# Kernel optimization log

Hardware: AMD Instinct MI355X
Metric: run time of the kernel (lower is better)

Reference implementation:

```python
import jax, jax.numpy as jnp
import numpy as np

N, K, P = 40000, 32, 15
C = 128            # output_feature_dim (kpconv in/out channels)
H_POS, D_POS = 64, 256
H_AGG, D_PROC = 256, 256
RADIUS = 1.0
KP_EXTENT = RADIUS / (P ** (1.0 / 3.0) - 1.0) * 1.5
SLOPE = 0.01       # nn.LeakyReLU default
EPS = 1e-5         # BatchNorm1d default eps


def _lin(key, din, dout):
    k1, k2 = jax.random.split(key)
    lim = 1.0 / np.sqrt(din)
    w = jax.random.uniform(k1, (din, dout), minval=-lim, maxval=lim, dtype=jnp.float32)
    b = jax.random.uniform(k2, (dout,), minval=-lim, maxval=lim, dtype=jnp.float32)
    return w, b


def _bn(x, g, b):
    # BatchNorm1d in training mode: biased batch statistics
    m = jnp.mean(x, axis=0)
    v = jnp.var(x, axis=0)
    return (x - m) * jax.lax.rsqrt(v + EPS) * g + b


def _lrelu(x):
    return jnp.where(x >= 0, x, SLOPE * x)


def setup_inputs() -> dict:
    key = jax.random.key(0)
    ks = jax.random.split(key, 16)
    inp = {}
    inp['points'] = jax.random.normal(ks[0], (N, 3), dtype=jnp.float32) * 10.0
    inp['covariances'] = jax.random.normal(ks[1], (N, 9), dtype=jnp.float32)
    inp['neighbors_index'] = jax.random.randint(ks[2], (N, K), 0, N)
    inp['pre_w'], inp['pre_b'] = _lin(ks[3], 9, C)
    inp['pre_bn_g'] = jnp.ones((C,), jnp.float32); inp['pre_bn_b'] = jnp.zeros((C,), jnp.float32)
    kp = jax.random.normal(ks[4], (P, 3), dtype=jnp.float32)
    kp = kp / jnp.linalg.norm(kp, axis=1, keepdims=True)
    inp['kernel_points'] = kp * jax.random.uniform(ks[5], (P, 1), dtype=jnp.float32) * RADIUS
    inp['kp_weights'] = jax.random.normal(ks[6], (P, C, C), dtype=jnp.float32) * (1.0 / np.sqrt(P * C))
    inp['pos_w1'], inp['pos_b1'] = _lin(ks[7], 3, H_POS)
    inp['pos_bn1_g'] = jnp.ones((H_POS,), jnp.float32); inp['pos_bn1_b'] = jnp.zeros((H_POS,), jnp.float32)
    inp['pos_w2'], inp['pos_b2'] = _lin(ks[8], H_POS, D_POS)
    inp['pos_bn2_g'] = jnp.ones((D_POS,), jnp.float32); inp['pos_bn2_b'] = jnp.zeros((D_POS,), jnp.float32)
    inp['agg_w1'], inp['agg_b1'] = _lin(ks[9], C, H_AGG)
    inp['agg_bn1_g'] = jnp.ones((H_AGG,), jnp.float32); inp['agg_bn1_b'] = jnp.zeros((H_AGG,), jnp.float32)
    inp['agg_w2'], inp['agg_b2'] = _lin(ks[10], H_AGG, D_PROC)
    inp['agg_bn2_g'] = jnp.ones((D_PROC,), jnp.float32); inp['agg_bn2_b'] = jnp.zeros((D_PROC,), jnp.float32)
    inp['keep_w1'], inp['keep_b1'] = _lin(ks[11], D_PROC, D_PROC // 4)
    inp['keep_bn_g'] = jnp.ones((D_PROC // 4,), jnp.float32); inp['keep_bn_b'] = jnp.zeros((D_PROC // 4,), jnp.float32)
    inp['keep_w2'], inp['keep_b2'] = _lin(ks[12], D_PROC // 4, 1)
    du = D_PROC + D_POS
    inp['uniq_w1'], inp['uniq_b1'] = _lin(ks[13], du, du // 4)
    inp['uniq_bn_g'] = jnp.ones((du // 4,), jnp.float32); inp['uniq_bn_b'] = jnp.zeros((du // 4,), jnp.float32)
    inp['uniq_w2'], inp['uniq_b2'] = _lin(ks[14], du // 4, 1)
    return inp


def reference(points, covariances, neighbors_index,
              pre_w, pre_b, pre_bn_g, pre_bn_b,
              kernel_points, kp_weights,
              pos_w1, pos_b1, pos_bn1_g, pos_bn1_b,
              pos_w2, pos_b2, pos_bn2_g, pos_bn2_b,
              agg_w1, agg_b1, agg_bn1_g, agg_bn1_b,
              agg_w2, agg_b2, agg_bn2_g, agg_bn2_b,
              keep_w1, keep_b1, keep_bn_g, keep_bn_b, keep_w2, keep_b2,
              uniq_w1, uniq_b1, uniq_bn_g, uniq_bn_b, uniq_w2, uniq_b2):
    # preactivation on 9-dim flattened covariances
    features = _lrelu(_bn(covariances @ pre_w + pre_b, pre_bn_g, pre_bn_b))  # [N, C]

    # ---- rigid KPConv (linear influence, sum aggregation, shadow point at index N) ----
    s_pad = jnp.concatenate([points, jnp.full((1, 3), 1e6, points.dtype)], axis=0)
    x_pad = jnp.concatenate([features, jnp.zeros((1, C), features.dtype)], axis=0)
    nb = s_pad[neighbors_index] - points[:, None, :]                          # [N, K, 3]
    # squared distances to kernel points without materializing [N,K,P,3]
    sq = (jnp.sum(nb * nb, -1)[:, :, None]
          + jnp.sum(kernel_points * kernel_points, -1)[None, None, :]
          - 2.0 * jnp.einsum('nkd,pd->nkp', nb, kernel_points))               # [N, K, P]
    infl = jnp.maximum(1.0 - jnp.sqrt(jnp.maximum(sq, 0.0)) / KP_EXTENT, 0.0)  # [N, K, P]
    nx = x_pad[neighbors_index]                                               # [N, K, C]
    weighted = jnp.einsum('nkp,nkc->npc', infl, nx)                           # [N, P, C]
    conv = jnp.einsum('npc,pcd->nd', weighted, kp_weights)                    # [N, C]
    # density normalization: count non-shadow neighbors
    nnum = jnp.maximum(jnp.sum(jnp.sum(nx, -1) > 0.0, axis=-1), 1)
    kpconv_feature = conv / nnum[:, None].astype(conv.dtype)

    # position embedding MLP
    pos = _lrelu(_bn(points @ pos_w1 + pos_b1, pos_bn1_g, pos_bn1_b))
    pos = _lrelu(_bn(pos @ pos_w2 + pos_b2, pos_bn2_g, pos_bn2_b))            # [N, 256]

    # feature aggregation MLP
    agg = _lrelu(_bn(kpconv_feature @ agg_w1 + agg_b1, agg_bn1_g, agg_bn1_b))
    agg = _lrelu(_bn(agg @ agg_w2 + agg_b2, agg_bn2_g, agg_bn2_b))            # [N, 256]

    # heads
    kh = _lrelu(_bn(agg @ keep_w1 + keep_b1, keep_bn_g, keep_bn_b))
    match_score = jax.nn.sigmoid((kh @ keep_w2 + keep_b2).ravel())
    u_in = jnp.concatenate([pos, agg], axis=1)                                # [N, 512]
    uh = _lrelu(_bn(u_in @ uniq_w1 + uniq_b1, uniq_bn_g, uniq_bn_b))
    unique_score = jax.nn.sigmoid((uh @ uniq_w2 + uniq_b2).ravel())
    return match_score, unique_score, neighbors_index
```

## Files before the change

kernel.cpp:

```cpp
#include <hip/hip_runtime.h>
#include <math.h>


#define NPTS 40000
#define KNB  32
#define PKP  15
#define SLOPE 0.01f
#define BNEPS 1e-5f
#define INV_N (1.0f/40000.0f)

typedef __attribute__((ext_vector_type(8))) short bf16x8;
typedef __attribute__((ext_vector_type(4))) float f32x4;

__device__ __forceinline__ float lrelu(float x){ return x >= 0.0f ? x : SLOPE*x; }
__device__ __forceinline__ unsigned short f2bf(float f){
  unsigned int b = __float_as_uint(f);
  b += 0x7fffu + ((b>>16)&1u);
  return (unsigned short)(b>>16);
}
__device__ __forceinline__ float bf2f(unsigned short u){
  return __uint_as_float(((unsigned int)u)<<16);
}


__global__ __launch_bounds__(256) void k_prep(
    const float* __restrict__ kpw,  const float* __restrict__ pw2,
    const float* __restrict__ aw1,  const float* __restrict__ aw2,
    const float* __restrict__ kw1,  const float* __restrict__ uw1,
    unsigned short* __restrict__ wT,
    unsigned short* __restrict__ posw2B, unsigned short* __restrict__ uw1B,
    const float* __restrict__ cov, const float* __restrict__ pts,
    float* __restrict__ mom){
  __shared__ float sM[63];
  int bid = blockIdx.x, tid = threadIdx.x;
  if (bid < 1728){
    int i = bid*256 + tid;
    const float* src; int K, N, off, li;
    if      (i < 245760){ src=kpw; K=1920; N=128; off=0;      li=i; }
    else if (i < 262144){ src=pw2; K=64;   N=256; off=245760; li=i-245760; }
    else if (i < 294912){ src=aw1; K=128;  N=256; off=262144; li=i-262144; }
    else if (i < 360448){ src=aw2; K=256;  N=256; off=294912; li=i-294912; }
    else if (i < 376832){ src=kw1; K=256;  N=64;  off=360448; li=i-360448; }
    else                { src=uw1; K=512;  N=128; off=376832; li=i-376832; }
    int k = li / N, n = li - k*N;
    wT[(size_t)off + (size_t)n*K + k] = f2bf(src[li]);
  } else if (bid < 1920){
    int i2 = (bid-1728)*256 + tid;
    if (i2 < 16384){
      int f = i2 >> 9, l = (i2 >> 3) & 63, j = i2 & 7;
      int cf = f >> 1, m = f & 1;
      int k = m*32 + (l>>4)*8 + j;
      int col = cf*16 + (l & 15);
      posw2B[i2] = f2bf(pw2[k*256 + col]);
    } else {
      int i3 = i2 - 16384;
      int f = i3 >> 9, l = (i3 >> 3) & 63, j = i3 & 7;
      int cf = f >> 3, m = f & 7;
      int k = m*32 + (l>>4)*8 + j;
      int c = cf*16 + (l & 15);
      uw1B[i3] = f2bf(uw1[k*128 + c]);
    }
  } else {
    int lane = tid & 63;
    int row = (bid-1920)*256 + tid;
    if (tid < 63) sM[tid] = 0.0f;
    __syncthreads();
    float c9[9] = {0,0,0,0,0,0,0,0,0};
    float p3[3] = {0,0,0};
    if (row < NPTS){
      #pragma unroll
      for (int i = 0; i < 9; ++i) c9[i] = cov[row*9+i];
      #pragma unroll
      for (int i = 0; i < 3; ++i) p3[i] = pts[row*3+i];
    }
    float vals[63];
    int q = 0;
    #pragma unroll
    for (int i = 0; i < 9; ++i) vals[q++] = c9[i];
    #pragma unroll
    for (int i = 0; i < 9; ++i)
      #pragma unroll
      for (int j = i; j < 9; ++j) vals[q++] = c9[i]*c9[j];
    #pragma unroll
    for (int i = 0; i < 3; ++i) vals[q++] = p3[i];
    #pragma unroll
    for (int i = 0; i < 3; ++i)
      #pragma unroll
      for (int j = i; j < 3; ++j) vals[q++] = p3[i]*p3[j];
    #pragma unroll
    for (int qq = 0; qq < 63; ++qq){
      float v = vals[qq];
      #pragma unroll
      for (int o = 32; o; o >>= 1) v += __shfl_down(v, o, 64);
      if (lane == 0) atomicAdd(&sM[qq], v);
    }
    __syncthreads();
    if (tid < 63) atomicAdd(&mom[tid], sM[tid]);
  }
}

__global__ __launch_bounds__(256) void k_bnsetup(
    const float* __restrict__ preW, const float* __restrict__ preB,
    const float* __restrict__ preG, const float* __restrict__ preBB,
    const float* __restrict__ posW1, const float* __restrict__ posB1,
    const float* __restrict__ posG1, const float* __restrict__ posBB1,
    float* __restrict__ stats){
  int tid = threadIdx.x;
  const float* mom = stats + 2320;
  if (tid < 128){
    int c = tid;
    float wv[9];
    #pragma unroll
    for (int i = 0; i < 9; ++i) wv[i] = preW[i*128+c];
    float b = preB[c];
    float mw = 0.0f;
    #pragma unroll
    for (int i = 0; i < 9; ++i) mw += wv[i]*mom[i];
    mw *= INV_N;
    float quad = 0.0f;
    for (int i = 0; i < 9; ++i)
      for (int j = 0; j < 9; ++j){
        int ii = i < j ? i : j, jj = i < j ? j : i;
        quad += wv[i]*wv[j]*mom[9 + ii*9 - (ii*(ii-1))/2 + (jj-ii)];
      }
    quad *= INV_N;
    float mean = mw + b;
    float var = quad + 2.0f*b*mw + b*b - mean*mean;
    float sc = preG[c]*rsqrtf(var+BNEPS);
    stats[c]     = sc;
    stats[128+c] = preBB[c] - mean*sc + sc*b;
  } else if (tid < 192){
    int c = tid - 128;
    float w0 = posW1[c], w1 = posW1[64+c], w2 = posW1[128+c];
    float b = posB1[c];
    const float* pm = mom + 54;
    const float* pM = mom + 57;
    float mw = (w0*pm[0] + w1*pm[1] + w2*pm[2])*INV_N;
    float quad = (w0*w0*pM[0] + w1*w1*pM[3] + w2*w2*pM[5]
               + 2.0f*(w0*w1*pM[1] + w0*w2*pM[2] + w1*w2*pM[4]))*INV_N;
    float mean = mw + b;
    float var = quad + 2.0f*b*mw + b*b - mean*mean;
    float sc = posG1[c]*rsqrtf(var+BNEPS);
    stats[256+c] = sc;
    stats[320+c] = posBB1[c] - mean*sc + sc*b;
  }
}

__global__ __launch_bounds__(256) void k_feat(
    const float* __restrict__ cov, const float* __restrict__ preW,
    const float* __restrict__ stats, unsigned short* __restrict__ feat,
    float* __restrict__ fsum){
  int tid = threadIdx.x;
  int lane = tid & 63;
  int wv = (blockIdx.x*256 + tid) >> 6;
  int nw = gridDim.x*4;
  int c0 = lane, c1 = lane + 64;
  float w0[9], w1[9];
  #pragma unroll
  for (int i = 0; i < 9; ++i){ w0[i] = preW[i*128+c0]; w1[i] = preW[i*128+c1]; }
  float s0 = stats[c0], h0 = stats[128+c0];
  float s1 = stats[c1], h1 = stats[128+c1];
  for (int n = wv; n < NPTS; n += nw){
    float p0 = 0.0f, p1 = 0.0f;
    #pragma unroll
    for (int i = 0; i < 9; ++i){
      float x = cov[n*9+i];
      p0 += x*w0[i]; p1 += x*w1[i];
    }
    float f0 = lrelu(s0*p0 + h0);
    float f1 = lrelu(s1*p1 + h1);
    feat[(size_t)n*128 + c0] = f2bf(f0);
    feat[(size_t)n*128 + c1] = f2bf(f1);
    float t = f0 + f1;
    #pragma unroll
    for (int o = 32; o; o >>= 1) t += __shfl_down(t, o, 64);
    if (lane == 0) fsum[n] = t;
  }
}

__global__ __launch_bounds__(256) void k_scan(
    const float* __restrict__ pts, const int* __restrict__ nbr,
    const float* __restrict__ kp, const float* __restrict__ fsum,
    float* __restrict__ invn, int* __restrict__ list,
    int* __restrict__ gcount, float ext2){
  __shared__ float sKP[45];
  if (threadIdx.x < 45) sKP[threadIdx.x] = kp[threadIdx.x];
  __syncthreads();
  int wv   = (blockIdx.x*256 + threadIdx.x) >> 6;
  int lane = threadIdx.x & 63;
  int half = lane >> 5;
  int kk   = lane & 31;
  int n    = wv*2 + half;
  float px = pts[n*3+0], py = pts[n*3+1], pz = pts[n*3+2];
  int j = nbr[(size_t)n*KNB + kk];
  float nx = pts[j*3+0] - px;
  float ny = pts[j*3+1] - py;
  float nz = pts[j*3+2] - pz;
  float fs = fsum[j];
  bool anyp = false;
  #pragma unroll
  for (int p = 0; p < PKP; ++p){
    float dx = nx - sKP[p*3+0], dy = ny - sKP[p*3+1], dz = nz - sKP[p*3+2];
    anyp |= (dx*dx + dy*dy + dz*dz < ext2);
  }
  unsigned long long act  = __ballot(anyp);
  unsigned long long good = __ballot(fs > 0.0f);
  unsigned int actH  = half ? (unsigned int)(act  >> 32) : (unsigned int)act;
  unsigned int goodH = half ? (unsigned int)(good >> 32) : (unsigned int)good;
  if (kk == 0){
    int cnt = __popc(goodH);
    invn[n] = 1.0f / (float)(cnt < 1 ? 1 : cnt);
    if (actH){
      int pos = atomicAdd(gcount, 1);
      list[pos] = n;
    }
  }
}

__global__ __launch_bounds__(256) void k_conv_act(
    const float* __restrict__ pts, const int* __restrict__ nbr,
    const float* __restrict__ kp, const unsigned short* __restrict__ feat,
    const unsigned short* __restrict__ kpwT, const float* __restrict__ invn,
    const int* __restrict__ list, const int* __restrict__ gcount,
    unsigned short* __restrict__ kpfc, float ext2, float inv_ext){
  __shared__ float sW[PKP*128];
  __shared__ float sInfl[KNB*16];
  __shared__ unsigned int sPairP[KNB];
  __shared__ float sKP[45];
  __shared__ float sOut[128];
  __shared__ unsigned int sPmask, sPact;
  int tid = threadIdx.x;
  if (tid < 45) sKP[tid] = kp[tid];
  int cnt = *gcount;
  for (int it = blockIdx.x; it < cnt; it += gridDim.x){
    int n = list[it];
    if (tid == 0){ sPmask = 0u; sPact = 0u; }
    for (int i = tid; i < PKP*128; i += 256) sW[i] = 0.0f;
    __syncthreads();
    if (tid < KNB){
      int j = nbr[(size_t)n*KNB + tid];
      float nx = pts[j*3+0] - pts[n*3+0];
      float ny = pts[j*3+1] - pts[n*3+1];
      float nz = pts[j*3+2] - pts[n*3+2];
      unsigned int pm = 0u;
      #pragma unroll
      for (int p = 0; p < PKP; ++p){
        float dx = nx - sKP[p*3+0], dy = ny - sKP[p*3+1], dz = nz - sKP[p*3+2];
        float d2 = dx*dx + dy*dy + dz*dz;
        float infl = 0.0f;
        if (d2 < ext2){ infl = 1.0f - sqrtf(d2)*inv_ext; pm |= (1u << p); }
        sInfl[tid*16 + p] = infl;
      }
      sPairP[tid] = pm;
      if (pm){
        atomicOr(&sPact, 1u << tid);
        atomicOr(&sPmask, pm);
      }
    }
    __syncthreads();
    if (tid < 128){
      int c = tid;
      unsigned int m = sPact;
      while (m){
        int k = __ffs(m) - 1; m &= m - 1;
        int j = nbr[(size_t)n*KNB + k];
        float f = bf2f(feat[(size_t)j*128 + c]);
        unsigned int pp = sPairP[k];
        while (pp){
          int p = __ffs(pp) - 1; pp &= pp - 1;
          sW[p*128 + c] += sInfl[k*16 + p] * f;
        }
      }
    }
    __syncthreads();
    int d = tid & 127, h = tid >> 7;
    float acc = 0.0f;
    unsigned int pm = sPmask;
    while (pm){
      int p = __ffs(pm) - 1; pm &= pm - 1;
      const unsigned short* wp = kpwT + (size_t)d*1920 + p*128 + h*64;
      const float* wsrc = &sW[p*128 + h*64];
      #pragma unroll
      for (int c8 = 0; c8 < 8; ++c8){
        uint4 v = *(const uint4*)(wp + c8*8);
        unsigned int e[4] = {v.x, v.y, v.z, v.w};
        #pragma unroll
        for (int q = 0; q < 4; ++q){
          acc += wsrc[c8*8 + 2*q]     * bf2f((unsigned short)(e[q] & 0xffff));
          acc += wsrc[c8*8 + 2*q + 1] * bf2f((unsigned short)(e[q] >> 16));
        }
      }
    }
    if (h == 0) sOut[d] = acc;
    __syncthreads();
    if (h == 1) kpfc[(size_t)it*128 + d] = f2bf((sOut[d] + acc) * invn[n]);
    __syncthreads();
  }
}

__global__ __launch_bounds__(256) void k_posmom1(
    const float* __restrict__ pts, const float* __restrict__ posW1,
    const float* __restrict__ stats, float* __restrict__ partials){
  __shared__ float sXm[64][65];
  int tid = threadIdx.x;
  int ia[9], ja[9];
  bool va[9];
  #pragma unroll
  for (int q = 0; q < 9; ++q){
    int idx = tid + q*256;
    va[q] = (idx < 2144);
    if (!va[q]){ ia[q] = 0; ja[q] = 0; continue; }
    if (idx < 64){ ia[q] = idx; ja[q] = -1; }
    else {
      int t = idx - 64; int i = 0;
      while (t >= 64 - i){ t -= 64 - i; ++i; }
      ia[q] = i; ja[q] = i + t;
    }
  }
  int c = tid & 63, rg = tid >> 6;
  float w0 = posW1[c], w1v = posW1[64+c], w2v = posW1[128+c];
  float sc1 = stats[256+c], sh1 = stats[320+c];
  int base = blockIdx.x*64;
  for (int r = rg; r < 64; r += 4){
    int row = base + r;
    sXm[r][c] = lrelu(sc1*(pts[row*3+0]*w0 + pts[row*3+1]*w1v
                         + pts[row*3+2]*w2v) + sh1);
  }
  __syncthreads();
  #pragma unroll
  for (int q = 0; q < 9; ++q){
    if (!va[q]) continue;
    float a = 0.0f;
    if (ja[q] < 0){
      for (int r = 0; r < 64; ++r) a += sXm[r][ia[q]];
    } else {
      for (int r = 0; r < 64; ++r) a += sXm[r][ia[q]]*sXm[r][ja[q]];
    }
    partials[(size_t)blockIdx.x*2144 + tid + q*256] = a;
  }
}

__global__ __launch_bounds__(256) void k_posmom2(
    const float* __restrict__ partials, float* __restrict__ pm){
  int c = blockIdx.x*256 + threadIdx.x;
  if (c >= 2144) return;
  float a = 0.0f;
  for (int k = 0; k < 625; ++k) a += partials[(size_t)k*2144 + c];
  pm[c] = a;
}

__global__ __launch_bounds__(256) void k_posbn2a(
    const float* __restrict__ pm, const float* __restrict__ posW2,
    float* __restrict__ U){
  __shared__ float sRow[64];
  int k = blockIdx.x;
  int tid = threadIdx.x;
  if (tid < 64){
    int i = k < tid ? k : tid, j = k < tid ? tid : k;
    int tri = i*64 - (i*(i-1))/2 + (j - i);
    sRow[tid] = pm[64 + tri];
  }
  __syncthreads();
  float a = 0.0f;
  for (int j = 0; j < 64; ++j) a += sRow[j]*posW2[j*256 + tid];
  U[k*256 + tid] = a;
}

__global__ __launch_bounds__(256) void k_posbn2b(
    const float* __restrict__ pm, const float* __restrict__ U,
    const float* __restrict__ posW2, const float* __restrict__ b2,
    const float* __restrict__ g2, const float* __restrict__ bb2,
    float* __restrict__ stats){
  int c = threadIdx.x;
  float mlin = 0.0f, quad = 0.0f;
  for (int k = 0; k < 64; ++k){
    float wkc = posW2[k*256 + c];
    mlin += wkc * pm[k];
    quad += wkc * U[k*256 + c];
  }
  mlin *= INV_N; quad *= INV_N;
  float b = b2[c];
  float mean = mlin + b;
  float var = quad + 2.0f*b*mlin + b*b - mean*mean;
  float sc = g2[c]*rsqrtf(var + BNEPS);
  stats[384+c] = sc;
  stats[640+c] = bb2[c] - mean*sc + sc*b;
}

__global__ __launch_bounds__(256) void k_ufused(
    const float* __restrict__ pts, const float* __restrict__ posW1,
    const float* __restrict__ stats, const unsigned short* __restrict__ posw2B,
    const unsigned short* __restrict__ uw1B, const float* __restrict__ ub_eff,
    unsigned short* __restrict__ u1, float* __restrict__ st2048){
  __shared__ __align__(16) unsigned short sX[4096];
  __shared__ __align__(16) unsigned short sY[16384];
  __shared__ float sC[512];
  __shared__ float sSum[128], sSq[128];
  int tid = threadIdx.x;
  int row0 = blockIdx.x*64;
  int w = tid >> 6, l = tid & 63;
  for (int i = tid; i < 512; i += 256) sC[i] = stats[384 + i];
  if (tid < 128){ sSum[tid] = 0.0f; sSq[tid] = 0.0f; }
  {
    int c = tid & 63, rg = tid >> 6;
    float w0 = posW1[c], w1v = posW1[64+c], w2v = posW1[128+c];
    float sc1 = stats[256+c], sh1 = stats[320+c];
    for (int r = rg; r < 64; r += 4){
      int row = row0 + r;
      float f = lrelu(sc1*(pts[row*3+0]*w0 + pts[row*3+1]*w1v
                         + pts[row*3+2]*w2v) + sh1);
      *(unsigned short*)((char*)sX + ((r*128 + c*2) ^ ((r&7)<<4))) = f2bf(f);
    }
  }
  __syncthreads();
  int rowA = w*16 + (l & 15);
  bf16x8 af0 = *(const bf16x8*)((const char*)sX +
               ((rowA*128 + ((l>>4)*8)*2) ^ ((rowA&7)<<4)));
  bf16x8 af1 = *(const bf16x8*)((const char*)sX +
               ((rowA*128 + (32+(l>>4)*8)*2) ^ ((rowA&7)<<4)));
  #pragma unroll
  for (int c4 = 0; c4 < 4; ++c4){
    bf16x8 b0[4], b1[4];
    #pragma unroll
    for (int j = 0; j < 4; ++j){
      int cf = c4*4 + j;
      b0[j] = *(const bf16x8*)(posw2B + (size_t)(cf*2+0)*512 + l*8);
      b1[j] = *(const bf16x8*)(posw2B + (size_t)(cf*2+1)*512 + l*8);
    }
    f32x4 acc[4] = {};
    #pragma unroll
    for (int j = 0; j < 4; ++j){
      acc[j] = __builtin_amdgcn_mfma_f32_16x16x32_bf16(af0, b0[j], acc[j], 0,0,0);
      acc[j] = __builtin_amdgcn_mfma_f32_16x16x32_bf16(af1, b1[j], acc[j], 0,0,0);
    }
    #pragma unroll
    for (int j = 0; j < 4; ++j){
      int col = (c4*4+j)*16 + (l & 15);
      float sc = sC[col], sh = sC[256+col];
      #pragma unroll
      for (int r = 0; r < 4; ++r){
        int row = w*16 + (l >> 4)*4 + r;
        float y = lrelu(sc*acc[j][r] + sh);
        *(unsigned short*)((char*)sY + ((row*512 + col*2) ^ ((row&7)<<4))) = f2bf(y);
      }
    }
  }
  __syncthreads();
  #pragma unroll
  for (int c4 = 0; c4 < 2; ++c4){
    f32x4 acc[4] = {};
    #pragma unroll
    for (int m = 0; m < 8; ++m){
      int ka = m*32 + (l >> 4)*8;
      bf16x8 af = *(const bf16x8*)((const char*)sY +
                  ((rowA*512 + ka*2) ^ ((rowA&7)<<4)));
      bf16x8 bb[4];
      #pragma unroll
      for (int j = 0; j < 4; ++j)
        bb[j] = *(const bf16x8*)(uw1B + (size_t)((c4*4+j)*8+m)*512 + l*8);
      #pragma unroll
      for (int j = 0; j < 4; ++j)
        acc[j] = __builtin_amdgcn_mfma_f32_16x16x32_bf16(af, bb[j], acc[j], 0,0,0);
    }
    #pragma unroll
    for (int j = 0; j < 4; ++j){
      int colh = j*16 + (l & 15);
      int col  = c4*64 + colh;
      float bj = ub_eff[col];
      float cs = 0.0f, cq = 0.0f;
      #pragma unroll
      for (int r = 0; r < 4; ++r){
        int row = w*16 + (l >> 4)*4 + r;
        float v = acc[j][r] + bj;
        *(unsigned short*)((char*)sX + ((row*128 + colh*2) ^ ((row&7)<<4))) = f2bf(v);
        cs += v; cq += v*v;
      }
      atomicAdd(&sSum[col], cs);
      atomicAdd(&sSq[col],  cq);
    }
    __syncthreads();
    #pragma unroll
    for (int ps = 0; ps < 2; ++ps){
      int idx = ps*256 + tid;
      int row = idx >> 3, g = idx & 7;
      uint4 v = *(const uint4*)((const char*)sX + ((row*128 + g*16) ^ ((row&7)<<4)));
      *(uint4*)(u1 + (size_t)(row0+row)*128 + c4*64 + g*8) = v;
    }
    __syncthreads();
  }
  if (tid < 128){
    atomicAdd(&st2048[tid],     sSum[tid]);
    atomicAdd(&st2048[128+tid], sSq[tid]);
  }
}

__global__ __launch_bounds__(256) void k_rowgemm(
    const unsigned short* __restrict__ X,
    const float* __restrict__ st, const float* __restrict__ g,
    const float* __restrict__ bb, int K, int norm,
    const unsigned short* __restrict__ Wt, const float* __restrict__ bias,
    int NOUT, unsigned short* __restrict__ Y, float* __restrict__ statsOut,
    const int* __restrict__ list, const int* __restrict__ gcount){
  __shared__ float xs[256];
  __shared__ float sSc[256], sSh[256];
  int tid = threadIdx.x;
  if (norm && tid < K){
    float s = st[tid], q = st[K+tid];
    float mean = s*INV_N, var = q*INV_N - mean*mean;
    float sc = g[tid]*rsqrtf(var+BNEPS);
    sSc[tid] = sc; sSh[tid] = bb[tid] - mean*sc;
  }
  __syncthreads();
  int cnt = *gcount;
  float rs = 0.0f, rq = 0.0f;
  for (int it = blockIdx.x; it < cnt; it += gridDim.x){
    if (tid < K){
      float xv = bf2f(X[(size_t)it*K + tid]);
      if (norm) xv = lrelu(xv*sSc[tid] + sSh[tid]);
      xs[tid] = xv;
    }
    __syncthreads();
    if (tid < NOUT){
      float acc = bias[tid];
      const unsigned short* wp = Wt + (size_t)tid*K;
      for (int k8 = 0; k8 < K; k8 += 8){
        uint4 v = *(const uint4*)(wp + k8);
        unsigned int e[4] = {v.x, v.y, v.z, v.w};
        #pragma unroll
        for (int q = 0; q < 4; ++q){
          acc += xs[k8+2*q]   * bf2f((unsigned short)(e[q] & 0xffff));
          acc += xs[k8+2*q+1] * bf2f((unsigned short)(e[q] >> 16));
        }
      }
      Y[(size_t)it*NOUT + tid] = f2bf(acc);
      rs += acc; rq += acc*acc;
    }
    __syncthreads();
  }
  if (tid < NOUT && rs != 0.0f){
    atomicAdd(&statsOut[tid],      rs);
    atomicAdd(&statsOut[NOUT+tid], rq);
  }
}

__global__ __launch_bounds__(256) void k_const1(
    const float* __restrict__ b1, const float* __restrict__ g1,
    const float* __restrict__ bb1, const unsigned short* __restrict__ aggw2T,
    const float* __restrict__ b2, float* __restrict__ st896,
    float* __restrict__ v2, const int* __restrict__ gcount){
  __shared__ float sX[256];
  int tid = threadIdx.x;
  float fN = (float)(NPTS - *gcount);
  float s = b1[tid];
  st896[tid]     += fN*s;
  st896[256+tid] += fN*s*s;
  float su = st896[tid], sq = st896[256+tid];
  float mean = su*INV_N, var = sq*INV_N - mean*mean;
  float sc = g1[tid]*rsqrtf(var+BNEPS);
  sX[tid] = lrelu(s*sc + bb1[tid] - mean*sc);
  __syncthreads();
  float acc = b2[tid];
  const unsigned short* wp = aggw2T + (size_t)tid*256;
  for (int k8 = 0; k8 < 256; k8 += 8){
    uint4 v = *(const uint4*)(wp + k8);
    unsigned int e[4] = {v.x, v.y, v.z, v.w};
    #pragma unroll
    for (int q = 0; q < 4; ++q){
      acc += sX[k8+2*q]   * bf2f((unsigned short)(e[q] & 0xffff));
      acc += sX[k8+2*q+1] * bf2f((unsigned short)(e[q] >> 16));
    }
  }
  v2[tid] = acc;
}

__global__ __launch_bounds__(256) void k_const2(
    const float* __restrict__ v2, const float* __restrict__ g2,
    const float* __restrict__ bb2, const unsigned short* __restrict__ keepw1T,
    const float* __restrict__ kb1, const unsigned short* __restrict__ uw1T,
    const float* __restrict__ ub1, float* __restrict__ st1408,
    float* __restrict__ v3, float* __restrict__ ub_eff,
    const int* __restrict__ gcount){
  __shared__ float sX[256];
  int tid = threadIdx.x;
  float fN = (float)(NPTS - *gcount);
  float s = v2[tid];
  st1408[tid]     += fN*s;
  st1408[256+tid] += fN*s*s;
  float su = st1408[tid], sq = st1408[256+tid];
  float mean = su*INV_N, var = sq*INV_N - mean*mean;
  float sc = g2[tid]*rsqrtf(var+BNEPS);
  sX[tid] = lrelu(s*sc + bb2[tid] - mean*sc);
  __syncthreads();
  if (tid < 64){
    float acc = kb1[tid];
    const unsigned short* wp = keepw1T + (size_t)tid*256;
    for (int k8 = 0; k8 < 256; k8 += 8){
      uint4 v = *(const uint4*)(wp + k8);
      unsigned int e[4] = {v.x, v.y, v.z, v.w};
      #pragma unroll
      for (int q = 0; q < 4; ++q){
        acc += sX[k8+2*q]   * bf2f((unsigned short)(e[q] & 0xffff));
        acc += sX[k8+2*q+1] * bf2f((unsigned short)(e[q] >> 16));
      }
    }
    v3[tid] = acc;
  } else if (tid < 192){
    int c = tid - 64;
    float acc = ub1[c];
    const unsigned short* wp = uw1T + (size_t)c*512 + 256;
    for (int k8 = 0; k8 < 256; k8 += 8){
      uint4 v = *(const uint4*)(wp + k8);
      unsigned int e[4] = {v.x, v.y, v.z, v.w};
      #pragma unroll
      for (int q = 0; q < 4; ++q){
        acc += sX[k8+2*q]   * bf2f((unsigned short)(e[q] & 0xffff));
        acc += sX[k8+2*q+1] * bf2f((unsigned short)(e[q] >> 16));
      }
    }
    ub_eff[c] = acc;
  }
}

__global__ __launch_bounds__(64) void k_const3(
    const float* __restrict__ v3, const float* __restrict__ g3,
    const float* __restrict__ bb3, const float* __restrict__ kw2,
    const float* __restrict__ kb2, float* __restrict__ st1920,
    float* __restrict__ s3out, const int* __restrict__ gcount){
  int tid = threadIdx.x;
  float fN = (float)(NPTS - *gcount);
  float s = v3[tid];
  st1920[tid]    += fN*s;
  st1920[64+tid] += fN*s*s;
  float su = st1920[tid], sq = st1920[64+tid];
  float mean = su*INV_N, var = sq*INV_N - mean*mean;
  float sc = g3[tid]*rsqrtf(var+BNEPS);
  float h = lrelu(s*sc + bb3[tid] - mean*sc) * kw2[tid];
  #pragma unroll
  for (int o = 32; o; o >>= 1) h += __shfl_down(h, o, 64);
  if (tid == 0) s3out[0] = 1.0f/(1.0f + expf(-(h + kb2[0])));
}

__global__ __launch_bounds__(256) void k_udelta_keep(
    const unsigned short* __restrict__ a2c, const float* __restrict__ st1408,
    const float* __restrict__ g2, const float* __restrict__ bb2,
    const unsigned short* __restrict__ uw1T, const float* __restrict__ ub1,
    const float* __restrict__ ub_eff, unsigned short* __restrict__ u1,
    float* __restrict__ st2048,
    const unsigned short* __restrict__ k1c, const float* __restrict__ st1920,
    const float* __restrict__ g3, const float* __restrict__ b3,
    const float* __restrict__ kw2, const float* __restrict__ kb2,
    float* __restrict__ out,
    const int* __restrict__ list, const int* __restrict__ gcount){
  __shared__ float sX[256];
  __shared__ float sSc[256], sSh[256];
  int tid = threadIdx.x;
  int cnt = *gcount;
  if (blockIdx.x < 128){
    {
      float su = st1408[tid], sq = st1408[256+tid];
      float mean = su*INV_N, var = sq*INV_N - mean*mean;
      float sc = g2[tid]*rsqrtf(var+BNEPS);
      sSc[tid] = sc; sSh[tid] = bb2[tid] - mean*sc;
    }
    __syncthreads();
    for (int it = blockIdx.x; it < cnt; it += 128){
      int n = list[it];
      sX[tid] = lrelu(bf2f(a2c[(size_t)it*256 + tid])*sSc[tid] + sSh[tid]);
      __syncthreads();
      if (tid < 128){
        float acc = ub1[tid] - ub_eff[tid];
        const unsigned short* wp = uw1T + (size_t)tid*512 + 256;
        for (int k8 = 0; k8 < 256; k8 += 8){
          uint4 v = *(const uint4*)(wp + k8);
          unsigned int e[4] = {v.x, v.y, v.z, v.w};
          #pragma unroll
          for (int q = 0; q < 4; ++q){
            acc += sX[k8+2*q]   * bf2f((unsigned short)(e[q] & 0xffff));
            acc += sX[k8+2*q+1] * bf2f((unsigned short)(e[q] >> 16));
          }
        }
        float old = bf2f(u1[(size_t)n*128 + tid]);
        float neu = old + acc;
        u1[(size_t)n*128 + tid] = f2bf(neu);
        atomicAdd(&st2048[tid],     neu - old);
        atomicAdd(&st2048[128+tid], neu*neu - old*old);
      }
      __syncthreads();
    }
  } else {
    int lane = tid & 63;
    int wv = (blockIdx.x - 128)*4 + (tid >> 6);
    float su = st1920[lane], sq = st1920[64+lane];
    float mean = su*INV_N, var = sq*INV_N - mean*mean;
    float sc = g3[lane]*rsqrtf(var+BNEPS);
    float sh = b3[lane] - mean*sc;
    float w2v = kw2[lane];
    for (int it = wv; it < cnt; it += 128){
      float h = lrelu(bf2f(k1c[(size_t)it*64 + lane])*sc + sh) * w2v;
      #pragma unroll
      for (int o = 32; o; o >>= 1) h += __shfl_down(h, o, 64);
      if (lane == 0) out[list[it]] = 1.0f/(1.0f + expf(-(h + kb2[0])));
    }
  }
}

__global__ __launch_bounds__(256) void k_uhead_out(
    const unsigned short* __restrict__ u1, const float* __restrict__ st2048,
    const float* __restrict__ g, const float* __restrict__ b,
    const float* __restrict__ w2, const float* __restrict__ b2,
    const int* __restrict__ nbr, const float* __restrict__ s3p,
    float* __restrict__ out){
  __shared__ float sSc[128], sSh[128], sW2[128];
  int tid = threadIdx.x;
  if (blockIdx.x >= 2500){
    int i = (blockIdx.x - 2500)*256 + tid;
    if (i < NPTS) out[i] = s3p[0];
    int4 v = ((const int4*)nbr)[i];
    ((float4*)(out + 2*NPTS))[i] =
        make_float4((float)v.x,(float)v.y,(float)v.z,(float)v.w);
    return;
  }
  if (tid < 128){
    float su = st2048[tid], sq = st2048[128+tid];
    float mean = su*INV_N, var = sq*INV_N - mean*mean;
    float sc = g[tid]*rsqrtf(var+BNEPS);
    sSc[tid] = sc; sSh[tid] = b[tid] - mean*sc;
    sW2[tid] = w2[tid];
  }
  __syncthreads();
  int lane = tid & 63, w = tid >> 6;
  for (int n = blockIdx.x*4 + w; n < NPTS; n += 10000){
    unsigned int v = *(const unsigned int*)(u1 + (size_t)n*128 + lane*2);
    int c0 = lane*2, c1 = c0 + 1;
    float h = lrelu(bf2f((unsigned short)(v & 0xffff))*sSc[c0] + sSh[c0])*sW2[c0]
            + lrelu(bf2f((unsigned short)(v >> 16))*sSc[c1] + sSh[c1])*sW2[c1];
    #pragma unroll
    for (int o = 32; o; o >>= 1) h += __shfl_down(h, o, 64);
    if (lane == 0) out[NPTS + n] = 1.0f/(1.0f + expf(-(h + b2[0])));
  }
}

extern "C" void kernel_launch(void* const* d_in, const int* in_sizes, int n_in,
                              void* d_out, int out_size, void* d_ws, size_t ws_size,
                              hipStream_t stream) {
  const float* pts    = (const float*)d_in[0];
  const float* cov    = (const float*)d_in[1];
  const int*   nbr    = (const int*)  d_in[2];
  const float* pre_w  = (const float*)d_in[3];
  const float* pre_b  = (const float*)d_in[4];
  const float* pre_g  = (const float*)d_in[5];
  const float* pre_bb = (const float*)d_in[6];
  const float* kp     = (const float*)d_in[7];
  const float* kpw    = (const float*)d_in[8];
  const float* pos_w1 = (const float*)d_in[9];
  const float* pos_b1 = (const float*)d_in[10];
  const float* pos_g1 = (const float*)d_in[11];
  const float* pos_bb1= (const float*)d_in[12];
  const float* pos_w2 = (const float*)d_in[13];
  const float* pos_b2 = (const float*)d_in[14];
  const float* pos_g2 = (const float*)d_in[15];
  const float* pos_bb2= (const float*)d_in[16];
  const float* agg_w1 = (const float*)d_in[17];
  const float* agg_b1 = (const float*)d_in[18];
  const float* agg_g1 = (const float*)d_in[19];
  const float* agg_bb1= (const float*)d_in[20];
  const float* agg_w2 = (const float*)d_in[21];
  const float* agg_b2 = (const float*)d_in[22];
  const float* agg_g2 = (const float*)d_in[23];
  const float* agg_bb2= (const float*)d_in[24];
  const float* keep_w1= (const float*)d_in[25];
  const float* keep_b1= (const float*)d_in[26];
  const float* keep_g = (const float*)d_in[27];
  const float* keep_bb= (const float*)d_in[28];
  const float* keep_w2= (const float*)d_in[29];
  const float* keep_b2= (const float*)d_in[30];
  const float* uniq_w1= (const float*)d_in[31];
  const float* uniq_b1= (const float*)d_in[32];
  const float* uniq_g = (const float*)d_in[33];
  const float* uniq_bb= (const float*)d_in[34];
  const float* uniq_w2= (const float*)d_in[35];
  const float* uniq_b2= (const float*)d_in[36];

  float* out = (float*)d_out;

  char* wsb = (char*)d_ws;
  size_t off = 0;
  float* stats = (float*)(wsb + off); off += 8192*4;
  int*   gcount = (int*)(stats + 2304);
  float* s3     = stats + 2305;
  float* mom    = stats + 2320;
  float* v2     = stats + 2384;
  float* v3     = stats + 2640;
  float* ub_eff = stats + 2704;
  float* pm     = stats + 2832;
  float* U      = (float*)(wsb + off); off += 16384*4;
  float* partials = (float*)(wsb + off); off += (size_t)625*2144*4;
  unsigned short* wT = (unsigned short*)(wsb + off); off += (size_t)442368*2;
  unsigned short* kpwT   = wT;
  unsigned short* aggw1T = wT + 262144;
  unsigned short* aggw2T = wT + 294912;
  unsigned short* keepw1T= wT + 360448;
  unsigned short* uniqw1T= wT + 376832;
  unsigned short* posw2B = (unsigned short*)(wsb + off); off += (size_t)16384*2;
  unsigned short* uw1B   = (unsigned short*)(wsb + off); off += (size_t)32768*2;
  float* fsum = (float*)(wsb + off); off += (size_t)NPTS*4;
  float* invn = (float*)(wsb + off); off += (size_t)NPTS*4;
  int*   list = (int*)  (wsb + off); off += (size_t)NPTS*4;
  unsigned short* feat = (unsigned short*)(wsb + off); off += (size_t)NPTS*128*2;
  unsigned short* kpfc = (unsigned short*)(wsb + off); off += (size_t)NPTS*128*2;
  unsigned short* a1c  = (unsigned short*)(wsb + off); off += (size_t)NPTS*256*2;
  unsigned short* a2c  = (unsigned short*)(wsb + off); off += (size_t)NPTS*256*2;
  unsigned short* k1c  = (unsigned short*)(wsb + off); off += (size_t)NPTS*64*2;
  unsigned short* u1   = (unsigned short*)(wsb + off); off += (size_t)NPTS*128*2;

  const double kpe = 1.0 / (cbrt(15.0) - 1.0) * 1.5;
  const float inv_ext = (float)(1.0 / kpe);
  const float ext2 = (float)(kpe * kpe);

  hipMemsetAsync(stats, 0, 2832*sizeof(float), stream);

  k_prep<<<2080, 256, 0, stream>>>(kpw, pos_w2, agg_w1, agg_w2, keep_w1,
                                   uniq_w1, wT, posw2B, uw1B, cov, pts, mom);
  k_bnsetup<<<1, 256, 0, stream>>>(pre_w, pre_b, pre_g, pre_bb,
                                   pos_w1, pos_b1, pos_g1, pos_bb1, stats);
  k_feat<<<2500, 256, 0, stream>>>(cov, pre_w, stats, feat, fsum);
  k_scan<<<5000, 256, 0, stream>>>(pts, nbr, kp, fsum, invn, list, gcount, ext2);
  k_conv_act<<<1024, 256, 0, stream>>>(pts, nbr, kp, feat, kpwT, invn,
                                       list, gcount, kpfc, ext2, inv_ext);

  k_posmom1<<<625, 256, 0, stream>>>(pts, pos_w1, stats, partials);
  k_posmom2<<<9, 256, 0, stream>>>(partials, pm);
  k_posbn2a<<<64, 256, 0, stream>>>(pm, pos_w2, U);
  k_posbn2b<<<1, 256, 0, stream>>>(pm, U, pos_w2, pos_b2, pos_g2, pos_bb2, stats);

  k_rowgemm<<<256, 256, 0, stream>>>(kpfc, nullptr, nullptr, nullptr, 128, 0,
                                     aggw1T, agg_b1, 256, a1c, stats + 896,
                                     list, gcount);
  k_const1<<<1, 256, 0, stream>>>(agg_b1, agg_g1, agg_bb1, aggw2T, agg_b2,
                                  stats + 896, v2, gcount);
  k_rowgemm<<<256, 256, 0, stream>>>(a1c, stats + 896, agg_g1, agg_bb1, 256, 1,
                                     aggw2T, agg_b2, 256, a2c, stats + 1408,
                                     list, gcount);
  k_const2<<<1, 256, 0, stream>>>(v2, agg_g2, agg_bb2, keepw1T, keep_b1,
                                  uniqw1T, uniq_b1, stats + 1408, v3, ub_eff,
                                  gcount);
  k_rowgemm<<<256, 256, 0, stream>>>(a2c, stats + 1408, agg_g2, agg_bb2, 256, 1,
                                     keepw1T, keep_b1, 64, k1c, stats + 1920,
                                     list, gcount);
  k_const3<<<1, 64, 0, stream>>>(v3, keep_g, keep_bb, keep_w2, keep_b2,
                                 stats + 1920, s3, gcount);

  k_ufused<<<625, 256, 0, stream>>>(pts, pos_w1, stats, posw2B, uw1B,
                                    ub_eff, u1, stats + 2048);
  k_udelta_keep<<<160, 256, 0, stream>>>(a2c, stats + 1408, agg_g2, agg_bb2,
                                         uniqw1T, uniq_b1, ub_eff, u1,
                                         stats + 2048, k1c, stats + 1920,
                                         keep_g, keep_bb, keep_w2, keep_b2,
                                         out, list, gcount);
  k_uhead_out<<<3750, 256, 0, stream>>>(u1, stats + 2048, uniq_g, uniq_bb,
                                        uniq_w2, uniq_b2, nbr, s3, out);
}
```

Before: 298.5 us.

## Make k_ufused wave-private: per-wave LDS tiles, register A-fragments, shuffle-reduced stats

Restructures the fused position-MLP/uniqueness GEMM kernel so each wave owns a private LDS tile, removing most block-level barriers. The first-layer features are computed directly into MFMA A-fragments in registers instead of staging through LDS. Column sums for batch-norm stats are reduced with wave shuffles and pushed straight to global atomics, dropping the shared-memory atomics. This shrinks LDS usage and may raise occupancy. The trade-off is more global atomics per block (one set per wave instead of one per block) and extra redundant ALU work per lane.

```diff
diff --git a/kernel.cpp b/kernel.cpp
--- a/kernel.cpp
+++ b/kernel.cpp
@@ -392,32 +392,27 @@
     const float* __restrict__ stats, const unsigned short* __restrict__ posw2B,
     const unsigned short* __restrict__ uw1B, const float* __restrict__ ub_eff,
     unsigned short* __restrict__ u1, float* __restrict__ st2048){
-  __shared__ __align__(16) unsigned short sX[4096];
-  __shared__ __align__(16) unsigned short sY[16384];
-  __shared__ float sC[512];
-  __shared__ float sSum[128], sSq[128];
+  __shared__ float sP[960];
+  __shared__ __align__(16) unsigned short sY[4][4096];
   int tid = threadIdx.x;
   int row0 = blockIdx.x*64;
   int w = tid >> 6, l = tid & 63;
-  for (int i = tid; i < 512; i += 256) sC[i] = stats[384 + i];
-  if (tid < 128){ sSum[tid] = 0.0f; sSq[tid] = 0.0f; }
-  {
-    int c = tid & 63, rg = tid >> 6;
-    float w0 = posW1[c], w1v = posW1[64+c], w2v = posW1[128+c];
-    float sc1 = stats[256+c], sh1 = stats[320+c];
-    for (int r = rg; r < 64; r += 4){
-      int row = row0 + r;
-      float f = lrelu(sc1*(pts[row*3+0]*w0 + pts[row*3+1]*w1v
-                         + pts[row*3+2]*w2v) + sh1);
-      *(unsigned short*)((char*)sX + ((r*128 + c*2) ^ ((r&7)<<4))) = f2bf(f);
-    }
-  }
+  for (int i = tid; i < 960; i += 256)
+    sP[i] = (i < 192) ? posW1[i] : (i < 832 ? stats[i + 64] : ub_eff[i - 832]);
   __syncthreads();
-  int rowA = w*16 + (l & 15);
-  bf16x8 af0 = *(const bf16x8*)((const char*)sX +
-               ((rowA*128 + ((l>>4)*8)*2) ^ ((rowA&7)<<4)));
-  bf16x8 af1 = *(const bf16x8*)((const char*)sX +
-               ((rowA*128 + (32+(l>>4)*8)*2) ^ ((rowA&7)<<4)));
+  unsigned short* myY = sY[w];
+  int g = l >> 4;
+  int arow = row0 + w*16 + (l & 15);
+  float px = pts[arow*3+0], py = pts[arow*3+1], pz = pts[arow*3+2];
+  bf16x8 af0, af1;
+  #pragma unroll
+  for (int j = 0; j < 8; ++j){
+    int c0 = g*8 + j, c1 = 32 + g*8 + j;
+    float x0 = lrelu(sP[192+c0]*(px*sP[c0] + py*sP[64+c0] + pz*sP[128+c0]) + sP[256+c0]);
+    float x1 = lrelu(sP[192+c1]*(px*sP[c1] + py*sP[64+c1] + pz*sP[128+c1]) + sP[256+c1]);
+    ((unsigned short*)&af0)[j] = f2bf(x0);
+    ((unsigned short*)&af1)[j] = f2bf(x1);
+  }
   #pragma unroll
   for (int c4 = 0; c4 < 4; ++c4){
     bf16x8 b0[4], b1[4];
@@ -436,61 +431,69 @@
     #pragma unroll
     for (int j = 0; j < 4; ++j){
       int col = (c4*4+j)*16 + (l & 15);
-      float sc = sC[col], sh = sC[256+col];
+      float sc = sP[320+col], sh = sP[576+col];
       #pragma unroll
       for (int r = 0; r < 4; ++r){
-        int row = w*16 + (l >> 4)*4 + r;
+        int lrow = g*4 + r;
         float y = lrelu(sc*acc[j][r] + sh);
-        *(unsigned short*)((char*)sY + ((row*512 + col*2) ^ ((row&7)<<4))) = f2bf(y);
-      }
-    }
-  }
-  __syncthreads();
+        *(unsigned short*)((char*)myY + ((lrow*512 + col*2) ^ ((lrow&7)<<4))) = f2bf(y);
+      }
+    }
+  }
+  bf16x8 afm[8];
+  {
+    int lrow = l & 15;
+    #pragma unroll
+    for (int m = 0; m < 8; ++m){
+      int k0 = m*32 + g*8;
+      afm[m] = *(const bf16x8*)((const char*)myY + ((lrow*512 + k0*2) ^ ((lrow&7)<<4)));
+    }
+  }
   #pragma unroll
   for (int c4 = 0; c4 < 2; ++c4){
     f32x4 acc[4] = {};
     #pragma unroll
     for (int m = 0; m < 8; ++m){
-      int ka = m*32 + (l >> 4)*8;
-      bf16x8 af = *(const bf16x8*)((const char*)sY +
-                  ((rowA*512 + ka*2) ^ ((rowA&7)<<4)));
       bf16x8 bb[4];
       #pragma unroll
       for (int j = 0; j < 4; ++j)
         bb[j] = *(const bf16x8*)(uw1B + (size_t)((c4*4+j)*8+m)*512 + l*8);
       #pragma unroll
       for (int j = 0; j < 4; ++j)
-        acc[j] = __builtin_amdgcn_mfma_f32_16x16x32_bf16(af, bb[j], acc[j], 0,0,0);
-    }
+        acc[j] = __builtin_amdgcn_mfma_f32_16x16x32_bf16(afm[m], bb[j], acc[j], 0,0,0);
+    }
+    float cs[4], cq[4];
     #pragma unroll
     for (int j = 0; j < 4; ++j){
       int colh = j*16 + (l & 15);
-      int col  = c4*64 + colh;
-      float bj = ub_eff[col];
-      float cs = 0.0f, cq = 0.0f;
+      float bj = sP[832 + c4*64 + colh];
+      cs[j] = 0.0f; cq[j] = 0.0f;
       #pragma unroll
       for (int r = 0; r < 4; ++r){
-        int row = w*16 + (l >> 4)*4 + r;
+        int lrow = g*4 + r;
         float v = acc[j][r] + bj;
-        *(unsigned short*)((char*)sX + ((row*128 + colh*2) ^ ((row&7)<<4))) = f2bf(v);
-        cs += v; cq += v*v;
-      }
-      atomicAdd(&sSum[col], cs);
-      atomicAdd(&sSq[col],  cq);
-    }
-    __syncthreads();
-    #pragma unroll
-    for (int ps = 0; ps < 2; ++ps){
-      int idx = ps*256 + tid;
-      int row = idx >> 3, g = idx & 7;
-      uint4 v = *(const uint4*)((const char*)sX + ((row*128 + g*16) ^ ((row&7)<<4)));
-      *(uint4*)(u1 + (size_t)(row0+row)*128 + c4*64 + g*8) = v;
-    }
-    __syncthreads();
-  }
-  if (tid < 128){
-    atomicAdd(&st2048[tid],     sSum[tid]);
-    atomicAdd(&st2048[128+tid], sSq[tid]);
+        *(unsigned short*)((char*)myY + (lrow*128 + colh*2)) = f2bf(v);
+        cs[j] += v; cq[j] += v*v;
+      }
+    }
+    #pragma unroll
+    for (int s = 0; s < 2; ++s){
+      int idx = l*2 + s;
+      int lrow = idx >> 3, q8 = idx & 7;
+      uint4 v = *(const uint4*)(myY + lrow*64 + q8*8);
+      *(uint4*)(u1 + (size_t)(row0 + w*16 + lrow)*128 + c4*64 + q8*8) = v;
+    }
+    #pragma unroll
+    for (int j = 0; j < 4; ++j){
+      float a = cs[j], b = cq[j];
+      a += __shfl_xor(a, 16, 64); a += __shfl_xor(a, 32, 64);
+      b += __shfl_xor(b, 16, 64); b += __shfl_xor(b, 32, 64);
+      if (l < 16){
+        int col = c4*64 + j*16 + l;
+        atomicAdd(&st2048[col],       a);
+        atomicAdd(&st2048[128 + col], b);
+      }
+    }
   }
 }
 
```

Measured after the change: 353.9 us. 18.5% more time.
